# Kernel optimization log

Measured on AMD Instinct MI355X. Metric: run time of the kernel, lower is better.

## Reference

```python
import math
import jax, jax.numpy as jnp
import numpy as np

H, PQ, PV, E, C, S, N = 12, 4, 8, 16, 128, 384, 512


def setup_inputs() -> dict:
    key = jax.random.key(0)
    ks = jax.random.split(key, 16)
    rn = lambda k, shape, scale=1.0: jax.random.normal(k, shape, jnp.float32) * scale
    single = rn(ks[0], (N, S))
    pair = rn(ks[1], (N, N, C))
    R, _ = jnp.linalg.qr(rn(ks[2], (N, 3, 3)))  # proper orthonormal frames
    t = rn(ks[3], (N, 3))
    w = 0.02
    return dict(
        single_representation=single,
        pair_representation=pair,
        rotations=R,
        translations=t,
        Wq=rn(ks[4], (H, S, E), w),
        Wk=rn(ks[5], (H, S, E), w),
        Wv=rn(ks[6], (H, S, E), w),
        Wqp=rn(ks[7], (H, PQ, S, 3), w),
        Wkp=rn(ks[8], (H, PQ, S, 3), w),
        Wvp=rn(ks[9], (H, PV, S, 3), w),
        Wb=rn(ks[10], (H, C), w),
        Wout=rn(ks[11], (H * (C + E + PV * 4), S), w),
        b_out=jnp.zeros((S,), jnp.float32),
        scale_head=jnp.ones((H,), jnp.float32),
    )


def _frame_apply(R, t, pts):
    # R:[N,3,3], t:[N,3], pts:[H,P,N,3] -> R_n @ p + t_n per residue n
    return jnp.einsum('nij,hpnj->hpni', R, pts) + t[None, None, :, :]


def reference(single_representation, pair_representation, rotations, translations,
              Wq, Wk, Wv, Wqp, Wkp, Wvp, Wb, Wout, b_out, scale_head):
    single, pair = single_representation, pair_representation
    n = single.shape[0]

    # --- sequence QK term ---
    q = jnp.einsum('nd,hde->hne', single, Wq)
    k = jnp.einsum('nd,hde->hne', single, Wk)
    w_single = math.sqrt(1.0 / E) * jnp.einsum('hne,hme->hnm', q, k)  # [H,N,N]

    # --- pair bias term ---
    w_pair = jnp.einsum('nmc,hc->hnm', pair, Wb)  # [H,N,N]

    # --- frame (3D point distance) term ---
    qp = jnp.einsum('nd,hpdk->hpnk', single, Wqp)  # [H,PQ,N,3]
    kp = jnp.einsum('nd,hpdk->hpnk', single, Wkp)
    lqp = _frame_apply(rotations, translations, qp)
    lkp = _frame_apply(rotations, translations, kp)
    diff = lqp[:, :, :, None, :] - lkp[:, :, None, :, :]   # [H,PQ,N,N,3]
    sqd = jnp.sum(diff * diff, axis=(1, 4))                 # [H,N,N] (sum over points & xyz)
    w_frame = (-math.sqrt(1.0 / (18 * PQ))) * jax.nn.softplus(scale_head)[:, None, None] * sqd

    w = jax.nn.softmax(w_single + w_pair + w_frame, axis=-1)  # [H,N,N]

    # --- sequence value aggregation ---
    v = jnp.einsum('nd,hde->hne', single, Wv)
    att_single = jnp.einsum('hnm,hme->hne', w, v)             # [H,N,E]
    att_single = jnp.transpose(att_single, (1, 0, 2)).reshape(n, -1)

    # --- pair value aggregation (faithful to source: sums over query index too) ---
    colsum = jnp.sum(w, axis=1)                               # [H,N] = sum_a w[h,a,b]
    att_pair = jnp.einsum('hb,ibc->hic', colsum, pair)        # [H,N,C]
    att_pair = jnp.transpose(att_pair, (1, 0, 2)).reshape(n, -1)

    # --- 3D point value aggregation ---
    vp = jnp.einsum('nd,hpdk->hpnk', single, Wvp)             # [H,PV,N,3]
    lvp = _frame_apply(rotations, translations, vp)
    local_out = jnp.einsum('hnm,hpmk->hpnk', w, lvp)          # [H,PV,N,3]
    Rinv = jnp.swapaxes(rotations, -1, -2)                    # R^T
    tinv = -jnp.einsum('nij,nj->ni', Rinv, translations)      # -R^T t
    global_out = _frame_apply(Rinv, tinv, local_out)          # [H,PV,N,3]
    out_points = jnp.transpose(global_out, (2, 1, 0, 3)).reshape(n, -1)  # [N, PV*H*3]
    out_norm = jnp.linalg.norm(global_out, axis=-1)           # [H,PV,N]
    out_norm = jnp.transpose(out_norm, (2, 1, 0)).reshape(n, -1)         # [N, PV*H]

    att = jnp.concatenate([att_single, att_pair, out_points, out_norm], axis=-1)
    return att @ Wout + b_out
```

## Files before the change

### kernel.cpp

```cpp
#include <hip/hip_runtime.h>
#include <math.h>

#define NRES 512
#define HH 12
#define PQn 4
#define PVn 8
#define En 16
#define Cn 128
#define Sn 384
#define ATT_COLS 2112

#define OFF_Q    0
#define OFF_K    (OFF_Q   + HH*NRES*En)
#define OFF_V    (OFF_K   + HH*NRES*En)
#define OFF_LQP  (OFF_V   + HH*NRES*En)
#define OFF_LKP  (OFF_LQP + HH*NRES*12)
#define OFF_LVP  (OFF_LKP + HH*NRES*12)
#define OFF_CS   (OFF_LVP + HH*NRES*24)
#define OFF_ATT  (OFF_CS  + NRES*HH)
#define OFF_LG   (OFF_ATT + NRES*ATT_COLS)
#define OFF_PART OFF_LG
#define KSPLIT 16
#define KCHUNK (ATT_COLS/KSPLIT)
#define OROWS 8

__global__ __launch_bounds__(256) void ipa_proj(
    const float* __restrict__ single, const float* __restrict__ Rm,
    const float* __restrict__ tr,
    const float* __restrict__ Wq, const float* __restrict__ Wk,
    const float* __restrict__ Wv, const float* __restrict__ Wqp,
    const float* __restrict__ Wkp, const float* __restrict__ Wvp,
    float* __restrict__ ws)
{
  float* q   = ws + OFF_Q;  float* k   = ws + OFF_K;  float* v   = ws + OFF_V;
  float* lqp = ws + OFF_LQP; float* lkp = ws + OFF_LKP; float* lvp = ws + OFF_LVP;
  const int n0 = blockIdx.x * 8;
  const int g  = blockIdx.y;
  const int tid = threadIdx.x;
  __shared__ float sS[8][388];
  __shared__ float sR[8][9];
  __shared__ float sT[8][3];
  #pragma unroll
  for (int i = 0; i < 3; ++i) {
    int idx = i*256 + tid;
    int r = idx / 96, c4 = idx % 96;
    float4 val = *reinterpret_cast<const float4*>(single + (size_t)(n0 + r)*Sn + c4*4);
    *reinterpret_cast<float4*>(&sS[r][c4*4]) = val;
  }
  if (tid < 72)      sR[tid/9][tid%9] = Rm[(size_t)(n0 + tid/9)*9 + tid%9];
  else if (tid < 96) { int r = (tid-72)/3; sT[r][(tid-72)%3] = tr[(size_t)(n0+r)*3 + (tid-72)%3]; }
  __syncthreads();
  #pragma unroll
  for (int i = 0; i < 3; ++i) {
    int item = i*256 + tid;
    int nl = item & 7;
    int ul = item >> 3;
    int u  = g*96 + ul;
    const float* srow = sS[nl];
    if (u < 576) {
      int which = u/192, r = u%192, h = r>>4, e = r&15;
      const float* W = (which==0 ? Wq : which==1 ? Wk : Wv) + (size_t)h*Sn*En + e;
      float acc = 0.f;
      #pragma unroll 8
      for (int d = 0; d < Sn; ++d) acc = fmaf(srow[d], W[(size_t)d*En], acc);
      float* dst = (which==0 ? q : which==1 ? k : v);
      dst[((size_t)h*NRES + (n0+nl))*En + e] = acc;
    } else {
      int u2 = u - 576;
      const float* W; float* dst;
      if (u2 < 48)      { int h=u2>>2,     p=u2&3;      W = Wqp + (size_t)(h*PQn+p)*Sn*3; dst = lqp + ((size_t)h*NRES + (n0+nl))*12 + p*3; }
      else if (u2 < 96) { int h=(u2-48)>>2,p=(u2-48)&3; W = Wkp + (size_t)(h*PQn+p)*Sn*3; dst = lkp + ((size_t)h*NRES + (n0+nl))*12 + p*3; }
      else              { int h=(u2-96)>>3,p=(u2-96)&7; W = Wvp + (size_t)(h*PVn+p)*Sn*3; dst = lvp + ((size_t)h*NRES + (n0+nl))*24 + p*3; }
      float x0=0.f,x1=0.f,x2=0.f;
      #pragma unroll 4
      for (int d = 0; d < Sn; ++d) {
        float sv = srow[d];
        x0 = fmaf(sv, W[d*3+0], x0);
        x1 = fmaf(sv, W[d*3+1], x1);
        x2 = fmaf(sv, W[d*3+2], x2);
      }
      const float* R8 = sR[nl]; const float* T8 = sT[nl];
      dst[0] = R8[0]*x0 + R8[1]*x1 + R8[2]*x2 + T8[0];
      dst[1] = R8[3]*x0 + R8[4]*x1 + R8[5]*x2 + T8[1];
      dst[2] = R8[6]*x0 + R8[7]*x1 + R8[8]*x2 + T8[2];
    }
  }
}

__global__ __launch_bounds__(256) void ipa_logits(
    const float* __restrict__ pair, const float* __restrict__ Wb,
    const float* __restrict__ scale_head, float* __restrict__ ws)
{
  const float* q   = ws + OFF_Q;  const float* k   = ws + OFF_K;
  const float* lqp = ws + OFF_LQP; const float* lkp = ws + OFF_LKP;
  float* lg = ws + OFF_LG;
  const int n  = blockIdx.x;
  const int mt = blockIdx.y;
  const int tid = threadIdx.x;
  const int lane = tid & 63;
  const int wave = tid >> 6;
  const int h0 = wave*3;
  const int m0 = mt*64;

  __shared__ float tile[64*128];
  const float* src = pair + ((size_t)n*NRES + m0)*Cn;
  #pragma unroll
  for (int i = 0; i < 8; ++i) {
    int idx = i*256 + tid;
    int r = idx >> 5, cf = idx & 31;
    float4 val = *reinterpret_cast<const float4*>(src + (size_t)r*Cn + cf*4);
    *reinterpret_cast<float4*>(&tile[r*128 + ((cf ^ (r & 31)) << 2)]) = val;
  }
  __syncthreads();

  float p[3] = {0.f, 0.f, 0.f};
  #pragma unroll 8
  for (int c4 = 0; c4 < 32; ++c4) {
    float4 pv = *reinterpret_cast<const float4*>(&tile[lane*128 + ((c4 ^ (lane & 31)) << 2)]);
    float4 w0 = *reinterpret_cast<const float4*>(Wb + (h0+0)*Cn + c4*4);
    float4 w1 = *reinterpret_cast<const float4*>(Wb + (h0+1)*Cn + c4*4);
    float4 w2 = *reinterpret_cast<const float4*>(Wb + (h0+2)*Cn + c4*4);
    p[0] += pv.x*w0.x + pv.y*w0.y + pv.z*w0.z + pv.w*w0.w;
    p[1] += pv.x*w1.x + pv.y*w1.y + pv.z*w1.z + pv.w*w1.w;
    p[2] += pv.x*w2.x + pv.y*w2.y + pv.z*w2.z + pv.w*w2.w;
  }

  const int m = m0 + lane;
  #pragma unroll
  for (int i = 0; i < 3; ++i) {
    const int h = h0 + i;
    const float* qh = q + ((size_t)h*NRES + n)*En;
    const float* kh = k + ((size_t)h*NRES + m)*En;
    float qk = 0.f;
    #pragma unroll
    for (int e = 0; e < En; ++e) qk = fmaf(qh[e], kh[e], qk);
    const float* lq = lqp + ((size_t)h*NRES + n)*12;
    const float* lk = lkp + ((size_t)h*NRES + m)*12;
    float cross=0.f, Bm=0.f, An=0.f;
    #pragma unroll
    for (int jj = 0; jj < 12; ++jj) {
      float a = lq[jj], b = lk[jj];
      cross = fmaf(a, b, cross); Bm = fmaf(b, b, Bm); An = fmaf(a, a, An);
    }
    float gamma = 0.11785113019775793f * log1pf(__expf(scale_head[h]));
    lg[((size_t)h*NRES + n)*NRES + m] = p[i] + 0.25f*qk - gamma*(An + Bm - 2.f*cross);
  }
}

__global__ __launch_bounds__(256) void ipa_softmax(float* __restrict__ ws)
{
  float* lg = ws + OFF_LG;
  const int row  = blockIdx.x*4 + (threadIdx.x >> 6);
  const int lane = threadIdx.x & 63;
  float4* p = reinterpret_cast<float4*>(lg + (size_t)row*NRES);
  float4 x0 = p[lane];
  float4 x1 = p[64 + lane];
  float mx = fmaxf(fmaxf(fmaxf(x0.x,x0.y),fmaxf(x0.z,x0.w)),
                   fmaxf(fmaxf(x1.x,x1.y),fmaxf(x1.z,x1.w)));
  #pragma unroll
  for (int off = 32; off >= 1; off >>= 1) mx = fmaxf(mx, __shfl_xor(mx, off));
  x0.x = __expf(x0.x-mx); x0.y = __expf(x0.y-mx); x0.z = __expf(x0.z-mx); x0.w = __expf(x0.w-mx);
  x1.x = __expf(x1.x-mx); x1.y = __expf(x1.y-mx); x1.z = __expf(x1.z-mx); x1.w = __expf(x1.w-mx);
  float sum = x0.x+x0.y+x0.z+x0.w + x1.x+x1.y+x1.z+x1.w;
  #pragma unroll
  for (int off = 32; off >= 1; off >>= 1) sum += __shfl_xor(sum, off);
  const float inv = 1.f/sum;
  x0.x*=inv; x0.y*=inv; x0.z*=inv; x0.w*=inv;
  x1.x*=inv; x1.y*=inv; x1.z*=inv; x1.w*=inv;
  p[lane] = x0;
  p[64 + lane] = x1;
}

__global__ __launch_bounds__(256) void ipa_colsum(float* __restrict__ ws)
{
  const float* lg = ws + OFF_LG;
  float* cs = ws + OFF_CS;
  const int h = blockIdx.x, ac = blockIdx.y, tid = threadIdx.x;
  const float* base = lg + (size_t)h*NRES*NRES + (size_t)ac*64*NRES;
  float acc0 = 0.f, acc1 = 0.f;
  #pragma unroll 4
  for (int a = 0; a < 64; ++a) {
    acc0 += base[(size_t)a*NRES + tid];
    acc1 += base[(size_t)a*NRES + tid + 256];
  }
  atomicAdd(&cs[h*NRES + tid],       acc0);
  atomicAdd(&cs[h*NRES + tid + 256], acc1);
}

__global__ __launch_bounds__(256) void ipa_agg(
    const float* __restrict__ Rm, const float* __restrict__ tr,
    float* __restrict__ ws)
{
  const float* v   = ws + OFF_V;
  const float* lvp = ws + OFF_LVP;
  const float* lg  = ws + OFF_LG;
  float* att = ws + OFF_ATT;
  const int row  = blockIdx.x*4 + (threadIdx.x >> 6);
  const int lane = threadIdx.x & 63;
  const int h = row >> 9, n = row & 511;

  float acc[40];
  #pragma unroll
  for (int i = 0; i < 40; ++i) acc[i] = 0.f;

  const float* wrow = lg + (size_t)row*NRES;
  #pragma unroll 2
  for (int j = 0; j < 8; ++j) {
    const int m = j*64 + lane;
    const float wv = wrow[m];
    const float4* v4 = reinterpret_cast<const float4*>(v + ((size_t)h*NRES + m)*En);
    float4 a0=v4[0], a1=v4[1], a2=v4[2], a3=v4[3];
    acc[0]+=wv*a0.x; acc[1]+=wv*a0.y; acc[2]+=wv*a0.z; acc[3]+=wv*a0.w;
    acc[4]+=wv*a1.x; acc[5]+=wv*a1.y; acc[6]+=wv*a1.z; acc[7]+=wv*a1.w;
    acc[8]+=wv*a2.x; acc[9]+=wv*a2.y; acc[10]+=wv*a2.z; acc[11]+=wv*a2.w;
    acc[12]+=wv*a3.x; acc[13]+=wv*a3.y; acc[14]+=wv*a3.z; acc[15]+=wv*a3.w;
    const float4* l4 = reinterpret_cast<const float4*>(lvp + ((size_t)h*NRES + m)*24);
    #pragma unroll
    for (int t = 0; t < 6; ++t) {
      float4 b = l4[t];
      acc[16+4*t+0]+=wv*b.x; acc[16+4*t+1]+=wv*b.y;
      acc[16+4*t+2]+=wv*b.z; acc[16+4*t+3]+=wv*b.w;
    }
  }
  #pragma unroll
  for (int off = 32; off >= 1; off >>= 1) {
    #pragma unroll
    for (int i = 0; i < 40; ++i) acc[i] += __shfl_xor(acc[i], off);
  }
  if (lane == 0) {
    size_t ab = (size_t)n*ATT_COLS;
    float4* as = reinterpret_cast<float4*>(att + ab + h*En);
    as[0] = make_float4(acc[0],acc[1],acc[2],acc[3]);
    as[1] = make_float4(acc[4],acc[5],acc[6],acc[7]);
    as[2] = make_float4(acc[8],acc[9],acc[10],acc[11]);
    as[3] = make_float4(acc[12],acc[13],acc[14],acc[15]);
    const float R0=Rm[n*9+0],R1=Rm[n*9+1],R2=Rm[n*9+2],
                R3=Rm[n*9+3],R4=Rm[n*9+4],R5=Rm[n*9+5],
                R6=Rm[n*9+6],R7=Rm[n*9+7],R8=Rm[n*9+8];
    const float t0=tr[n*3+0], t1=tr[n*3+1], t2=tr[n*3+2];
    #pragma unroll
    for (int pp = 0; pp < 8; ++pp) {
      float d0 = acc[16+3*pp+0]-t0, d1 = acc[16+3*pp+1]-t1, d2 = acc[16+3*pp+2]-t2;
      float g0 = R0*d0 + R3*d1 + R6*d2;
      float g1 = R1*d0 + R4*d1 + R7*d2;
      float g2 = R2*d0 + R5*d1 + R8*d2;
      att[ab + 1728 + (pp*HH + h)*3 + 0] = g0;
      att[ab + 1728 + (pp*HH + h)*3 + 1] = g1;
      att[ab + 1728 + (pp*HH + h)*3 + 2] = g2;
      att[ab + 2016 + pp*HH + h] = sqrtf(g0*g0 + g1*g1 + g2*g2);
    }
  }
}

__global__ __launch_bounds__(256) void ipa_pairagg(
    const float* __restrict__ pair, float* __restrict__ ws)
{
  const float* cs = ws + OFF_CS;
  float* att = ws + OFF_ATT;
  const int i = blockIdx.x, tid = threadIdx.x;
  __shared__ float sCS[HH*NRES];
  __shared__ float4 sRed[8][HH][32];
  #pragma unroll
  for (int it = 0; it < 6; ++it) {
    int idx = it*256 + tid;
    reinterpret_cast<float4*>(sCS)[idx] = reinterpret_cast<const float4*>(cs)[idx];
  }
  __syncthreads();
  const int c4 = tid & 31, bg = tid >> 5;
  float4 acc[HH];
  #pragma unroll
  for (int h = 0; h < HH; ++h) acc[h] = make_float4(0.f,0.f,0.f,0.f);
  const float* prow = pair + (size_t)i*NRES*Cn;
  for (int b = bg; b < NRES; b += 8) {
    float4 pv = *reinterpret_cast<const float4*>(prow + (size_t)b*Cn + c4*4);
    #pragma unroll
    for (int h = 0; h < HH; ++h) {
      float w = sCS[h*NRES + b];
      acc[h].x = fmaf(w, pv.x, acc[h].x);
      acc[h].y = fmaf(w, pv.y, acc[h].y);
      acc[h].z = fmaf(w, pv.z, acc[h].z);
      acc[h].w = fmaf(w, pv.w, acc[h].w);
    }
  }
  #pragma unroll
  for (int h = 0; h < HH; ++h) sRed[bg][h][c4] = acc[h];
  __syncthreads();
  for (int s = 4; s >= 1; s >>= 1) {
    if (bg < s) {
      #pragma unroll
      for (int h = 0; h < HH; ++h) {
        float4 a = sRed[bg][h][c4], b2 = sRed[bg+s][h][c4];
        a.x+=b2.x; a.y+=b2.y; a.z+=b2.z; a.w+=b2.w;
        sRed[bg][h][c4] = a;
      }
    }
    __syncthreads();
  }
  if (bg == 0) {
    size_t base = (size_t)i*ATT_COLS + 192;
    #pragma unroll
    for (int h = 0; h < HH; ++h)
      *reinterpret_cast<float4*>(att + base + h*Cn + c4*4) = sRed[0][h][c4];
  }
}

__global__ __launch_bounds__(384) void ipa_outp(
    const float* __restrict__ att, const float* __restrict__ Wout,
    float* __restrict__ ws)
{
  float* partial = ws + OFF_PART;
  const int rb = blockIdx.x;
  const int ks = blockIdx.y;
  const int s  = threadIdx.x;
  const int n0 = rb*OROWS;
  const int j0 = ks*KCHUNK;

  float acc[OROWS];
  #pragma unroll
  for (int r = 0; r < OROWS; ++r) acc[r] = 0.f;

  for (int jg = 0; jg < KCHUNK/4; ++jg) {
    const int j = j0 + jg*4;
    float w0 = Wout[(size_t)(j+0)*Sn + s];
    float w1 = Wout[(size_t)(j+1)*Sn + s];
    float w2 = Wout[(size_t)(j+2)*Sn + s];
    float w3 = Wout[(size_t)(j+3)*Sn + s];
    #pragma unroll
    for (int r = 0; r < OROWS; ++r) {
      float4 av = *reinterpret_cast<const float4*>(att + (size_t)(n0+r)*ATT_COLS + j);
      acc[r] = fmaf(av.x, w0, acc[r]);
      acc[r] = fmaf(av.y, w1, acc[r]);
      acc[r] = fmaf(av.z, w2, acc[r]);
      acc[r] = fmaf(av.w, w3, acc[r]);
    }
  }
  #pragma unroll
  for (int r = 0; r < OROWS; ++r)
    partial[((size_t)ks*NRES + n0 + r)*Sn + s] = acc[r];
}

__global__ __launch_bounds__(384) void ipa_outred(
    const float* __restrict__ b_out, float* __restrict__ ws,
    float* __restrict__ out)
{
  const float* partial = ws + OFF_PART;
  const int n = blockIdx.x, s = threadIdx.x;
  float a = b_out[s];
  #pragma unroll
  for (int ks = 0; ks < KSPLIT; ++ks)
    a += partial[((size_t)ks*NRES + n)*Sn + s];
  out[(size_t)n*Sn + s] = a;
}

extern "C" void kernel_launch(void* const* d_in, const int* in_sizes, int n_in,
                              void* d_out, int out_size, void* d_ws, size_t ws_size,
                              hipStream_t stream) {
  const float* single = (const float*)d_in[0];
  const float* pair   = (const float*)d_in[1];
  const float* Rm     = (const float*)d_in[2];
  const float* tr     = (const float*)d_in[3];
  const float* Wq     = (const float*)d_in[4];
  const float* Wk     = (const float*)d_in[5];
  const float* Wv     = (const float*)d_in[6];
  const float* Wqp    = (const float*)d_in[7];
  const float* Wkp    = (const float*)d_in[8];
  const float* Wvp    = (const float*)d_in[9];
  const float* Wb     = (const float*)d_in[10];
  const float* Wout   = (const float*)d_in[11];
  const float* b_out  = (const float*)d_in[12];
  const float* scale_head = (const float*)d_in[13];
  float* ws  = (float*)d_ws;
  float* out = (float*)d_out;

  hipMemsetAsync(ws + OFF_CS, 0, NRES*HH*sizeof(float), stream);
  ipa_proj   <<<dim3(64, 8),  256, 0, stream>>>(single, Rm, tr, Wq, Wk, Wv, Wqp, Wkp, Wvp, ws);
  ipa_logits <<<dim3(NRES, 8),256, 0, stream>>>(pair, Wb, scale_head, ws);
  ipa_softmax<<<dim3(HH*NRES/4), 256, 0, stream>>>(ws);
  ipa_colsum <<<dim3(HH, 8),  256, 0, stream>>>(ws);
  ipa_agg    <<<dim3(HH*NRES/4), 256, 0, stream>>>(Rm, tr, ws);
  ipa_pairagg<<<dim3(NRES),   256, 0, stream>>>(pair, ws);
  ipa_outp   <<<dim3(NRES/OROWS, KSPLIT), 384, 0, stream>>>(ws + OFF_ATT, Wout, ws);
  ipa_outred <<<dim3(NRES),   384, 0, stream>>>(b_out, ws, out);
}
```

Baseline: 272.0 us.

## Compute pair bias for all heads per thread directly from global memory

The pair-bias part of the logits kernel no longer stages a 64x128 pair tile in shared memory behind a barrier. Each group of four lanes now reads one pair row straight from global memory as float4s, accumulates all 12 heads, and combines the partial sums with wave shuffles. Each lane then keeps three heads for the q·k and point-distance terms, which changes the thread-to-(m,h) mapping and the store pattern. The softplus is also switched to __logf(1+__expf), which is cheaper but less accurate; the per-thread register footprint and the Wb load count go up.

Result: slower. 314.4 us (+15.6%).

```diff
diff --git a/kernel.cpp b/kernel.cpp
--- a/kernel.cpp
+++ b/kernel.cpp
@@ -94,41 +94,47 @@
   const float* q   = ws + OFF_Q;  const float* k   = ws + OFF_K;
   const float* lqp = ws + OFF_LQP; const float* lkp = ws + OFF_LKP;
   float* lg = ws + OFF_LG;
-  const int n  = blockIdx.x;
-  const int mt = blockIdx.y;
-  const int tid = threadIdx.x;
-  const int lane = tid & 63;
-  const int wave = tid >> 6;
-  const int h0 = wave*3;
-  const int m0 = mt*64;
-
-  __shared__ float tile[64*128];
-  const float* src = pair + ((size_t)n*NRES + m0)*Cn;
-  #pragma unroll
-  for (int i = 0; i < 8; ++i) {
-    int idx = i*256 + tid;
-    int r = idx >> 5, cf = idx & 31;
-    float4 val = *reinterpret_cast<const float4*>(src + (size_t)r*Cn + cf*4);
-    *reinterpret_cast<float4*>(&tile[r*128 + ((cf ^ (r & 31)) << 2)]) = val;
-  }
-  __syncthreads();
-
-  float p[3] = {0.f, 0.f, 0.f};
-  #pragma unroll 8
-  for (int c4 = 0; c4 < 32; ++c4) {
-    float4 pv = *reinterpret_cast<const float4*>(&tile[lane*128 + ((c4 ^ (lane & 31)) << 2)]);
-    float4 w0 = *reinterpret_cast<const float4*>(Wb + (h0+0)*Cn + c4*4);
-    float4 w1 = *reinterpret_cast<const float4*>(Wb + (h0+1)*Cn + c4*4);
-    float4 w2 = *reinterpret_cast<const float4*>(Wb + (h0+2)*Cn + c4*4);
-    p[0] += pv.x*w0.x + pv.y*w0.y + pv.z*w0.z + pv.w*w0.w;
-    p[1] += pv.x*w1.x + pv.y*w1.y + pv.z*w1.z + pv.w*w1.w;
-    p[2] += pv.x*w2.x + pv.y*w2.y + pv.z*w2.z + pv.w*w2.w;
-  }
-
-  const int m = m0 + lane;
+  const int n    = blockIdx.x;
+  const int lane = threadIdx.x & 63;
+  const int wave = threadIdx.x >> 6;
+  const int r    = lane >> 2;
+  const int cq   = lane & 3;
+  const int m    = blockIdx.y*64 + wave*16 + r;
+
+  const float* prow = pair + ((size_t)n*NRES + m)*Cn;
+  float acc[HH];
+  #pragma unroll
+  for (int h = 0; h < HH; ++h) acc[h] = 0.f;
+
+  #pragma unroll
+  for (int jg = 0; jg < 8; ++jg) {
+    const int c4 = jg*4 + cq;
+    float4 pv = *reinterpret_cast<const float4*>(prow + c4*4);
+    const float* wbb = Wb + c4*4;
+    #pragma unroll
+    for (int h = 0; h < HH; ++h) {
+      float4 wb = *reinterpret_cast<const float4*>(wbb + h*Cn);
+      acc[h] = fmaf(pv.x, wb.x, acc[h]);
+      acc[h] = fmaf(pv.y, wb.y, acc[h]);
+      acc[h] = fmaf(pv.z, wb.z, acc[h]);
+      acc[h] = fmaf(pv.w, wb.w, acc[h]);
+    }
+  }
+  #pragma unroll
+  for (int h = 0; h < HH; ++h) {
+    acc[h] += __shfl_xor(acc[h], 1);
+    acc[h] += __shfl_xor(acc[h], 2);
+  }
+  float a0, a1, a2;
+  if      (cq == 0) { a0 = acc[0]; a1 = acc[1];  a2 = acc[2];  }
+  else if (cq == 1) { a0 = acc[3]; a1 = acc[4];  a2 = acc[5];  }
+  else if (cq == 2) { a0 = acc[6]; a1 = acc[7];  a2 = acc[8];  }
+  else              { a0 = acc[9]; a1 = acc[10]; a2 = acc[11]; }
+  float pb[3] = {a0, a1, a2};
+
   #pragma unroll
   for (int i = 0; i < 3; ++i) {
-    const int h = h0 + i;
+    const int h = 3*cq + i;
     const float* qh = q + ((size_t)h*NRES + n)*En;
     const float* kh = k + ((size_t)h*NRES + m)*En;
     float qk = 0.f;
@@ -136,14 +142,14 @@
     for (int e = 0; e < En; ++e) qk = fmaf(qh[e], kh[e], qk);
     const float* lq = lqp + ((size_t)h*NRES + n)*12;
     const float* lk = lkp + ((size_t)h*NRES + m)*12;
-    float cross=0.f, Bm=0.f, An=0.f;
+    float cross = 0.f, Bm = 0.f, An = 0.f;
     #pragma unroll
     for (int jj = 0; jj < 12; ++jj) {
       float a = lq[jj], b = lk[jj];
       cross = fmaf(a, b, cross); Bm = fmaf(b, b, Bm); An = fmaf(a, a, An);
     }
-    float gamma = 0.11785113019775793f * log1pf(__expf(scale_head[h]));
-    lg[((size_t)h*NRES + n)*NRES + m] = p[i] + 0.25f*qk - gamma*(An + Bm - 2.f*cross);
+    float gamma = 0.11785113019775793f * __logf(1.f + __expf(scale_head[h]));
+    lg[((size_t)h*NRES + n)*NRES + m] = pb[i] + 0.25f*qk - gamma*(An + Bm - 2.f*cross);
   }
 }
 
```
